# Kernel optimization log

Hardware: AMD Instinct MI355X
Metric: run time of the kernel (lower is better)

## Reference

```python
import jax, jax.numpy as jnp
import numpy as np

B, C, H, W = 8, 64, 256, 256


def setup_inputs() -> dict:
    key = jax.random.key(0)
    ks = jax.random.split(key, 7)
    return {
        "x": jax.random.normal(ks[0], (B, C, H, W), dtype=jnp.float32),
        "query_w": jax.random.normal(ks[1], (C, W, W), dtype=jnp.float32),
        "key_w": jax.random.normal(ks[2], (C, W, W), dtype=jnp.float32),
        "var_w": jax.random.normal(ks[3], (C, W, W), dtype=jnp.float32),
        "query_b": jax.random.normal(ks[4], (C, H, W), dtype=jnp.float32),
        "key_b": jax.random.normal(ks[5], (C, H, W), dtype=jnp.float32),
        "var_b": jax.random.normal(ks[6], (C, H, W), dtype=jnp.float32),
    }


def reference(x, query_w, key_w, var_w, query_b, key_b, var_b):
    # mode == 'horizontal': per-channel right-matmul over the W axis.
    # x: [B,C,H,W], *_w: [C,W,W] (broadcast over batch), *_b: [C,H,W].
    q = jnp.einsum("bchw,cwv->bchv", x, query_w) + query_b
    k = jnp.einsum("bchw,cwv->bchv", x, key_w) + key_b
    v = jnp.einsum("bchw,cwv->bchv", x, var_w) + var_b
    return jax.nn.softmax(q * k, axis=-1) * v
```

## Files before the change

kernel.cpp:

```cpp
#include <hip/hip_runtime.h>
#include <math.h>


#define Bn 8
#define Cn 64
#define Hn 256
#define Wn 256

typedef _Float16 f16x8 __attribute__((ext_vector_type(8)));
typedef _Float16 f16x4 __attribute__((ext_vector_type(4)));
typedef float    f32x16 __attribute__((ext_vector_type(16)));

#define MFMA(a, b, c) __builtin_amdgcn_mfma_f32_32x32x16_f16((a), (b), (c), 0, 0, 0)

#define LDS_ALO 2048
#define LDS_B   4096
#define LDS_SM  36864

__global__ __launch_bounds__(256, 2) void axile_attn_mfma3(
    const float* __restrict__ x,
    const float* __restrict__ wq,
    const float* __restrict__ wk,
    const float* __restrict__ wv,
    const float* __restrict__ bq,
    const float* __restrict__ bk,
    const float* __restrict__ bv,
    float* __restrict__ out)
{
    __shared__ __align__(16) char lds[38400];

    const int tid  = threadIdx.x;
    const int ncol = tid >> 6;
    const int lane = tid & 63;
    const int h    = lane >> 5;
    const int l31  = lane & 31;

    const int blk = blockIdx.x;
    const int c   = blk & 63;
    const int j   = blk >> 6;
    const int b   = j >> 2;
    const int h0  = (j & 3) * 64;

    const float* xbase = x + ((size_t)(b * Cn + c) * Hn + h0) * Wn;
    const float* w_q = wq + (size_t)c * Wn * Wn;
    const float* w_k = wk + (size_t)c * Wn * Wn;
    const float* w_v = wv + (size_t)c * Wn * Wn;

    const int n    = tid;
    const int ntW  = n >> 5;
    const int nl   = n & 31;
    const int am    = tid >> 2;
    const int akq   = tid & 3;
    const int amt   = am >> 5;
    const int alc   = ((akq >> 1) << 5) | (am & 31);
    const int aboff = (akq & 1) * 8;

    f32x16 accq[2][2], acck[2][2];
#pragma unroll
    for (int mt = 0; mt < 2; ++mt)
#pragma unroll
        for (int nt = 0; nt < 2; ++nt)
#pragma unroll
            for (int r = 0; r < 16; ++r) {
                accq[mt][nt][r] = 0.f;
                acck[mt][nt][r] = 0.f;
            }

    for (int kt = 0; kt < 16; ++kt) {
        const int k0 = kt * 16;
        __syncthreads();
#pragma unroll
        for (int mat = 0; mat < 2; ++mat) {
            const float* Wp = mat ? w_k : w_q;
            float w16[16];
#pragma unroll
            for (int r = 0; r < 16; ++r)
                w16[r] = Wp[(size_t)(k0 + r) * Wn + n];
            char* dplane = lds + LDS_B + (mat * 2) * 8192 + ntW * 1024;
#pragma unroll
            for (int h2 = 0; h2 < 2; ++h2) {
                f16x8 hi8, lo8;
#pragma unroll
                for (int e = 0; e < 8; ++e) {
                    const float wv_ = w16[h2 * 8 + e];
                    _Float16 hv = (_Float16)wv_;
                    hi8[e] = hv;
                    lo8[e] = (_Float16)(wv_ - (float)hv);
                }
                const int fo = ((h2 << 5) | nl) * 16;
                *(f16x8*)(dplane + fo) = hi8;
                *(f16x8*)(dplane + 8192 + fo) = lo8;
            }
        }
        {
            const float4 xx = *(const float4*)(xbase + (size_t)am * Wn + k0 + akq * 4);
            f16x4 hi4, lo4;
            _Float16 t0 = (_Float16)xx.x; hi4[0] = t0; lo4[0] = (_Float16)(xx.x - (float)t0);
            _Float16 t1 = (_Float16)xx.y; hi4[1] = t1; lo4[1] = (_Float16)(xx.y - (float)t1);
            _Float16 t2 = (_Float16)xx.z; hi4[2] = t2; lo4[2] = (_Float16)(xx.z - (float)t2);
            _Float16 t3 = (_Float16)xx.w; hi4[3] = t3; lo4[3] = (_Float16)(xx.w - (float)t3);
            *(f16x4*)(lds + amt * 1024 + alc * 16 + aboff) = hi4;
            *(f16x4*)(lds + LDS_ALO + amt * 1024 + alc * 16 + aboff) = lo4;
        }
        __syncthreads();

        f16x8 ah[2], al[2];
#pragma unroll
        for (int mt = 0; mt < 2; ++mt) {
            ah[mt] = *(const f16x8*)(lds + mt * 1024 + lane * 16);
            al[mt] = *(const f16x8*)(lds + LDS_ALO + mt * 1024 + lane * 16);
        }
#pragma unroll
        for (int nt = 0; nt < 2; ++nt) {
            const int ntile = ncol * 2 + nt;
            const char* bb = lds + LDS_B + ntile * 1024 + lane * 16;
            f16x8 bqh = *(const f16x8*)(bb + 0 * 8192);
            f16x8 bql = *(const f16x8*)(bb + 1 * 8192);
            f16x8 bkh = *(const f16x8*)(bb + 2 * 8192);
            f16x8 bkl = *(const f16x8*)(bb + 3 * 8192);
#pragma unroll
            for (int mt = 0; mt < 2; ++mt) {
                accq[mt][nt] = MFMA(ah[mt], bqh, accq[mt][nt]);
                accq[mt][nt] = MFMA(al[mt], bqh, accq[mt][nt]);
                accq[mt][nt] = MFMA(ah[mt], bql, accq[mt][nt]);
                acck[mt][nt] = MFMA(ah[mt], bkh, acck[mt][nt]);
                acck[mt][nt] = MFMA(al[mt], bkh, acck[mt][nt]);
                acck[mt][nt] = MFMA(ah[mt], bkl, acck[mt][nt]);
            }
        }
    }

    float* part    = (float*)(lds + LDS_SM);
    float* combmax = (float*)(lds + LDS_SM + 1024);
    float* combsum = (float*)(lds + LDS_SM + 1280);

#pragma unroll
    for (int mt = 0; mt < 2; ++mt)
#pragma unroll
        for (int nt = 0; nt < 2; ++nt)
#pragma unroll
            for (int r = 0; r < 16; ++r) {
                const int rl = (r & 3) + 8 * (r >> 2) + 4 * h;
                const int hh = h0 + mt * 32 + rl;
                const int vv = ncol * 64 + nt * 32 + l31;
                const size_t bidx = ((size_t)c * Hn + hh) * Wn + vv;
                const float qv = accq[mt][nt][r] + bq[bidx];
                const float kv = acck[mt][nt][r] + bk[bidx];
                accq[mt][nt][r] = qv * kv;
            }

#pragma unroll
    for (int mt = 0; mt < 2; ++mt)
#pragma unroll
        for (int r = 0; r < 16; ++r) {
            float m2 = fmaxf(accq[mt][0][r], accq[mt][1][r]);
#pragma unroll
            for (int off = 16; off > 0; off >>= 1)
                m2 = fmaxf(m2, __shfl_xor(m2, off, 64));
            if ((lane & 15) == r && ((lane >> 4) & 1) == mt) {
                const int rl  = (r & 3) + 8 * (r >> 2) + 4 * h;
                const int row = mt * 32 + rl;
                part[row * 4 + ncol] = m2;
            }
        }
    __syncthreads();
    if (tid < 64)
        combmax[tid] = fmaxf(fmaxf(part[tid * 4 + 0], part[tid * 4 + 1]),
                             fmaxf(part[tid * 4 + 2], part[tid * 4 + 3]));
    __syncthreads();

#pragma unroll
    for (int mt = 0; mt < 2; ++mt)
#pragma unroll
        for (int r = 0; r < 16; ++r) {
            const int rl  = (r & 3) + 8 * (r >> 2) + 4 * h;
            const int row = mt * 32 + rl;
            const float mx = combmax[row];
            const float e0 = __expf(accq[mt][0][r] - mx);
            const float e1 = __expf(accq[mt][1][r] - mx);
            accq[mt][0][r] = e0;
            accq[mt][1][r] = e1;
            float ps = e0 + e1;
#pragma unroll
            for (int off = 16; off > 0; off >>= 1)
                ps += __shfl_xor(ps, off, 64);
            if ((lane & 15) == r && ((lane >> 4) & 1) == mt)
                part[row * 4 + ncol] = ps;
        }
    __syncthreads();
    if (tid < 64)
        combsum[tid] = (part[tid * 4 + 0] + part[tid * 4 + 1]) +
                       (part[tid * 4 + 2] + part[tid * 4 + 3]);

    f32x16 accv[2][2];
#pragma unroll
    for (int mt = 0; mt < 2; ++mt)
#pragma unroll
        for (int nt = 0; nt < 2; ++nt)
#pragma unroll
            for (int r = 0; r < 16; ++r)
                accv[mt][nt][r] = 0.f;

    for (int kt = 0; kt < 16; ++kt) {
        const int k0 = kt * 16;
        __syncthreads();
        {
            float w16[16];
#pragma unroll
            for (int r = 0; r < 16; ++r)
                w16[r] = w_v[(size_t)(k0 + r) * Wn + n];
            char* dplane = lds + LDS_B + ntW * 1024;
#pragma unroll
            for (int h2 = 0; h2 < 2; ++h2) {
                f16x8 hi8;
#pragma unroll
                for (int e = 0; e < 8; ++e)
                    hi8[e] = (_Float16)w16[h2 * 8 + e];
                *(f16x8*)(dplane + ((h2 << 5) | nl) * 16) = hi8;
            }
        }
        {
            const float4 xx = *(const float4*)(xbase + (size_t)am * Wn + k0 + akq * 4);
            f16x4 hi4;
            hi4[0] = (_Float16)xx.x;
            hi4[1] = (_Float16)xx.y;
            hi4[2] = (_Float16)xx.z;
            hi4[3] = (_Float16)xx.w;
            *(f16x4*)(lds + amt * 1024 + alc * 16 + aboff) = hi4;
        }
        __syncthreads();

        f16x8 ah[2];
#pragma unroll
        for (int mt = 0; mt < 2; ++mt)
            ah[mt] = *(const f16x8*)(lds + mt * 1024 + lane * 16);
#pragma unroll
        for (int nt = 0; nt < 2; ++nt) {
            const int ntile = ncol * 2 + nt;
            f16x8 bvh = *(const f16x8*)(lds + LDS_B + ntile * 1024 + lane * 16);
#pragma unroll
            for (int mt = 0; mt < 2; ++mt)
                accv[mt][nt] = MFMA(ah[mt], bvh, accv[mt][nt]);
        }
    }

    float* obase = out + ((size_t)(b * Cn + c) * Hn) * Wn;
#pragma unroll
    for (int mt = 0; mt < 2; ++mt)
#pragma unroll
        for (int r = 0; r < 16; ++r) {
            const int rl  = (r & 3) + 8 * (r >> 2) + 4 * h;
            const int row = mt * 32 + rl;
            const float inv = 1.0f / combsum[row];
            const int hh = h0 + row;
#pragma unroll
            for (int nt = 0; nt < 2; ++nt) {
                const int vv = ncol * 64 + nt * 32 + l31;
                const size_t bidx = ((size_t)c * Hn + hh) * Wn + vv;
                const float vx = accv[mt][nt][r] + bv[bidx];
                obase[(size_t)hh * Wn + vv] = accq[mt][nt][r] * vx * inv;
            }
        }
}

extern "C" void kernel_launch(void* const* d_in, const int* in_sizes, int n_in,
                              void* d_out, int out_size, void* d_ws, size_t ws_size,
                              hipStream_t stream) {
    (void)in_sizes; (void)n_in; (void)out_size; (void)d_ws; (void)ws_size;
    const float* x  = (const float*)d_in[0];
    const float* wq = (const float*)d_in[1];
    const float* wk = (const float*)d_in[2];
    const float* wv = (const float*)d_in[3];
    const float* bq = (const float*)d_in[4];
    const float* bk = (const float*)d_in[5];
    const float* bv = (const float*)d_in[6];
    float* out = (float*)d_out;

    dim3 grid(Bn * 4 * Cn);
    dim3 block(256);
    hipLaunchKernelGGL(axile_attn_mfma3, grid, block, 0, stream,
                       x, wq, wk, wv, bq, bk, bv, out);
}
```

Baseline: 534.0 us.

## Pre-split weights to fp16 hi/lo MFMA layout once, load via global_load_lds

```diff
diff --git a/kernel.cpp b/kernel.cpp
--- a/kernel.cpp
+++ b/kernel.cpp
@@ -1,5 +1,6 @@
 #include <hip/hip_runtime.h>
 #include <math.h>
+#include <stdint.h>
 
 
 #define Bn 8
@@ -11,11 +12,275 @@
 typedef _Float16 f16x4 __attribute__((ext_vector_type(4)));
 typedef float    f32x16 __attribute__((ext_vector_type(16)));
 
+typedef __attribute__((address_space(1))) const uint32_t gl_u32;
+typedef __attribute__((address_space(3))) uint32_t lds_u32;
+
 #define MFMA(a, b, c) __builtin_amdgcn_mfma_f32_32x32x16_f16((a), (b), (c), 0, 0, 0)
+
+#define WP_PLANE 4096
+#define WP_CKT   (5 * WP_PLANE)
+#define WS_NEED  ((size_t)Cn * 16 * WP_CKT * sizeof(_Float16))
 
 #define LDS_ALO 2048
 #define LDS_B   4096
 #define LDS_SM  36864
+
+__global__ __launch_bounds__(256) void convert_w(
+    const float* __restrict__ wq,
+    const float* __restrict__ wk,
+    const float* __restrict__ wv,
+    _Float16* __restrict__ wc)
+{
+    const int gid   = blockIdx.x * 256 + threadIdx.x;
+    const int lane  = gid & 63;
+    const int ntile = (gid >> 6) & 7;
+    const int kt    = (gid >> 9) & 15;
+    const int c     = gid >> 13;
+
+    const int k0  = kt * 16 + (lane >> 5) * 8;
+    const int col = ntile * 32 + (lane & 31);
+    const size_t cb = (size_t)c * Wn * Wn;
+
+    _Float16* dst = wc + ((size_t)c * 16 + kt) * WP_CKT;
+    const int fo  = ntile * 512 + lane * 8;
+
+    f16x8 qh, ql, kh, kl, vh;
+#pragma unroll
+    for (int e = 0; e < 8; ++e) {
+        const size_t idx = cb + (size_t)(k0 + e) * Wn + col;
+        const float q = wq[idx];
+        const float k = wk[idx];
+        const float v = wv[idx];
+        _Float16 qhv = (_Float16)q;
+        _Float16 khv = (_Float16)k;
+        qh[e] = qhv; ql[e] = (_Float16)(q - (float)qhv);
+        kh[e] = khv; kl[e] = (_Float16)(k - (float)khv);
+        vh[e] = (_Float16)v;
+    }
+    *(f16x8*)(dst + 0 * WP_PLANE + fo) = qh;
+    *(f16x8*)(dst + 1 * WP_PLANE + fo) = ql;
+    *(f16x8*)(dst + 2 * WP_PLANE + fo) = kh;
+    *(f16x8*)(dst + 3 * WP_PLANE + fo) = kl;
+    *(f16x8*)(dst + 4 * WP_PLANE + fo) = vh;
+}
+
+__global__ __launch_bounds__(256, 2) void axile_attn_mfma4(
+    const float* __restrict__ x,
+    const _Float16* __restrict__ wc,
+    const float* __restrict__ bq,
+    const float* __restrict__ bk,
+    const float* __restrict__ bv,
+    float* __restrict__ out)
+{
+    __shared__ __align__(16) char lds[38400];
+
+    const int tid  = threadIdx.x;
+    const int ncol = tid >> 6;
+    const int lane = tid & 63;
+    const int h    = lane >> 5;
+    const int l31  = lane & 31;
+
+    const int blk = blockIdx.x;
+    const int c   = blk & 63;
+    const int j   = blk >> 6;
+    const int b   = j >> 2;
+    const int h0  = (j & 3) * 64;
+
+    const float* xbase = x + ((size_t)(b * Cn + c) * Hn + h0) * Wn;
+    const _Float16* wcc = wc + (size_t)c * 16 * WP_CKT;
+
+    const int am    = tid >> 2;
+    const int akq   = tid & 3;
+    const int alc   = ((akq >> 1) << 5) | (am & 31);
+    const int aboff = (akq & 1) * 8;
+    const int amt   = am >> 5;
+
+    f32x16 accq[2][2], acck[2][2];
+#pragma unroll
+    for (int mt = 0; mt < 2; ++mt)
+#pragma unroll
+        for (int nt = 0; nt < 2; ++nt)
+#pragma unroll
+            for (int r = 0; r < 16; ++r) {
+                accq[mt][nt][r] = 0.f;
+                acck[mt][nt][r] = 0.f;
+            }
+
+    for (int kt = 0; kt < 16; ++kt) {
+        const int k0 = kt * 16;
+        __syncthreads();
+        {
+            const _Float16* srcp = wcc + (size_t)kt * WP_CKT + ncol * WP_PLANE + lane * 8;
+            char* ldsp = lds + LDS_B + ncol * 8192;
+#pragma unroll
+            for (int nt8 = 0; nt8 < 8; ++nt8)
+                __builtin_amdgcn_global_load_lds(
+                    (gl_u32*)(srcp + nt8 * 512), (lds_u32*)(ldsp + nt8 * 1024), 16, 0, 0);
+        }
+        {
+            const float4 xx = *(const float4*)(xbase + (size_t)am * Wn + k0 + akq * 4);
+            f16x4 hi4, lo4;
+            _Float16 t0 = (_Float16)xx.x; hi4[0] = t0; lo4[0] = (_Float16)(xx.x - (float)t0);
+            _Float16 t1 = (_Float16)xx.y; hi4[1] = t1; lo4[1] = (_Float16)(xx.y - (float)t1);
+            _Float16 t2 = (_Float16)xx.z; hi4[2] = t2; lo4[2] = (_Float16)(xx.z - (float)t2);
+            _Float16 t3 = (_Float16)xx.w; hi4[3] = t3; lo4[3] = (_Float16)(xx.w - (float)t3);
+            *(f16x4*)(lds + amt * 1024 + alc * 16 + aboff) = hi4;
+            *(f16x4*)(lds + LDS_ALO + amt * 1024 + alc * 16 + aboff) = lo4;
+        }
+        __syncthreads();
+
+        f16x8 ah[2], al[2];
+#pragma unroll
+        for (int mt = 0; mt < 2; ++mt) {
+            ah[mt] = *(const f16x8*)(lds + mt * 1024 + lane * 16);
+            al[mt] = *(const f16x8*)(lds + LDS_ALO + mt * 1024 + lane * 16);
+        }
+#pragma unroll
+        for (int nt = 0; nt < 2; ++nt) {
+            const int ntile = ncol * 2 + nt;
+            const char* bb = lds + LDS_B + ntile * 1024 + lane * 16;
+            f16x8 bqh = *(const f16x8*)(bb + 0 * 8192);
+            f16x8 bql = *(const f16x8*)(bb + 1 * 8192);
+            f16x8 bkh = *(const f16x8*)(bb + 2 * 8192);
+            f16x8 bkl = *(const f16x8*)(bb + 3 * 8192);
+#pragma unroll
+            for (int mt = 0; mt < 2; ++mt) {
+                accq[mt][nt] = MFMA(ah[mt], bqh, accq[mt][nt]);
+                accq[mt][nt] = MFMA(al[mt], bqh, accq[mt][nt]);
+                accq[mt][nt] = MFMA(ah[mt], bql, accq[mt][nt]);
+                acck[mt][nt] = MFMA(ah[mt], bkh, acck[mt][nt]);
+                acck[mt][nt] = MFMA(al[mt], bkh, acck[mt][nt]);
+                acck[mt][nt] = MFMA(ah[mt], bkl, acck[mt][nt]);
+            }
+        }
+    }
+
+    float* part    = (float*)(lds + LDS_SM);
+    float* combmax = (float*)(lds + LDS_SM + 1024);
+    float* combsum = (float*)(lds + LDS_SM + 1280);
+
+#pragma unroll
+    for (int mt = 0; mt < 2; ++mt)
+#pragma unroll
+        for (int nt = 0; nt < 2; ++nt)
+#pragma unroll
+            for (int r = 0; r < 16; ++r) {
+                const int rl = (r & 3) + 8 * (r >> 2) + 4 * h;
+                const int hh = h0 + mt * 32 + rl;
+                const int vv = ncol * 64 + nt * 32 + l31;
+                const size_t bidx = ((size_t)c * Hn + hh) * Wn + vv;
+                const float qv = accq[mt][nt][r] + bq[bidx];
+                const float kv = acck[mt][nt][r] + bk[bidx];
+                accq[mt][nt][r] = qv * kv;
+            }
+
+#pragma unroll
+    for (int mt = 0; mt < 2; ++mt)
+#pragma unroll
+        for (int r = 0; r < 16; ++r) {
+            float m2 = fmaxf(accq[mt][0][r], accq[mt][1][r]);
+#pragma unroll
+            for (int off = 16; off > 0; off >>= 1)
+                m2 = fmaxf(m2, __shfl_xor(m2, off, 64));
+            if ((lane & 15) == r && ((lane >> 4) & 1) == mt) {
+                const int rl  = (r & 3) + 8 * (r >> 2) + 4 * h;
+                part[(mt * 32 + rl) * 4 + ncol] = m2;
+            }
+        }
+    __syncthreads();
+    if (tid < 64)
+        combmax[tid] = fmaxf(fmaxf(part[tid * 4 + 0], part[tid * 4 + 1]),
+                             fmaxf(part[tid * 4 + 2], part[tid * 4 + 3]));
+    __syncthreads();
+
+#pragma unroll
+    for (int mt = 0; mt < 2; ++mt)
+#pragma unroll
+        for (int r = 0; r < 16; ++r) {
+            const int rl  = (r & 3) + 8 * (r >> 2) + 4 * h;
+            const int row = mt * 32 + rl;
+            const float mx = combmax[row];
+            const float e0 = __expf(accq[mt][0][r] - mx);
+            const float e1 = __expf(accq[mt][1][r] - mx);
+            accq[mt][0][r] = e0;
+            accq[mt][1][r] = e1;
+            float ps = e0 + e1;
+#pragma unroll
+            for (int off = 16; off > 0; off >>= 1)
+                ps += __shfl_xor(ps, off, 64);
+            if ((lane & 15) == r && ((lane >> 4) & 1) == mt)
+                part[row * 4 + ncol] = ps;
+        }
+    __syncthreads();
+    if (tid < 64)
+        combsum[tid] = (part[tid * 4 + 0] + part[tid * 4 + 1]) +
+                       (part[tid * 4 + 2] + part[tid * 4 + 3]);
+
+    f32x16 accv[2][2];
+#pragma unroll
+    for (int mt = 0; mt < 2; ++mt)
+#pragma unroll
+        for (int nt = 0; nt < 2; ++nt)
+#pragma unroll
+            for (int r = 0; r < 16; ++r)
+                accv[mt][nt][r] = 0.f;
+
+    for (int kt = 0; kt < 16; ++kt) {
+        const int k0 = kt * 16;
+        __syncthreads();
+        {
+            const _Float16* srcp = wcc + (size_t)kt * WP_CKT + 4 * WP_PLANE + lane * 8;
+#pragma unroll
+            for (int i = 0; i < 2; ++i) {
+                const int nt8 = ncol * 2 + i;
+                __builtin_amdgcn_global_load_lds(
+                    (gl_u32*)(srcp + nt8 * 512),
+                    (lds_u32*)(lds + LDS_B + nt8 * 1024), 16, 0, 0);
+            }
+        }
+        {
+            const float4 xx = *(const float4*)(xbase + (size_t)am * Wn + k0 + akq * 4);
+            f16x4 hi4;
+            hi4[0] = (_Float16)xx.x;
+            hi4[1] = (_Float16)xx.y;
+            hi4[2] = (_Float16)xx.z;
+            hi4[3] = (_Float16)xx.w;
+            *(f16x4*)(lds + amt * 1024 + alc * 16 + aboff) = hi4;
+        }
+        __syncthreads();
+
+        f16x8 ah[2];
+#pragma unroll
+        for (int mt = 0; mt < 2; ++mt)
+            ah[mt] = *(const f16x8*)(lds + mt * 1024 + lane * 16);
+#pragma unroll
+        for (int nt = 0; nt < 2; ++nt) {
+            const int ntile = ncol * 2 + nt;
+            f16x8 bvh = *(const f16x8*)(lds + LDS_B + ntile * 1024 + lane * 16);
+#pragma unroll
+            for (int mt = 0; mt < 2; ++mt)
+                accv[mt][nt] = MFMA(ah[mt], bvh, accv[mt][nt]);
+        }
+    }
+
+    float* obase = out + ((size_t)(b * Cn + c) * Hn) * Wn;
+#pragma unroll
+    for (int mt = 0; mt < 2; ++mt)
+#pragma unroll
+        for (int r = 0; r < 16; ++r) {
+            const int rl  = (r & 3) + 8 * (r >> 2) + 4 * h;
+            const int row = mt * 32 + rl;
+            const float inv = 1.0f / combsum[row];
+            const int hh = h0 + row;
+#pragma unroll
+            for (int nt = 0; nt < 2; ++nt) {
+                const int vv = ncol * 64 + nt * 32 + l31;
+                const size_t bidx = ((size_t)c * Hn + hh) * Wn + vv;
+                const float vx = accv[mt][nt][r] + bv[bidx];
+                obase[(size_t)hh * Wn + vv] = accq[mt][nt][r] * vx * inv;
+            }
+        }
+}
 
 __global__ __launch_bounds__(256, 2) void axile_attn_mfma3(
     const float* __restrict__ x,
@@ -28,24 +293,20 @@
     float* __restrict__ out)
 {
     __shared__ __align__(16) char lds[38400];
-
     const int tid  = threadIdx.x;
     const int ncol = tid >> 6;
     const int lane = tid & 63;
     const int h    = lane >> 5;
     const int l31  = lane & 31;
-
     const int blk = blockIdx.x;
     const int c   = blk & 63;
     const int j   = blk >> 6;
     const int b   = j >> 2;
     const int h0  = (j & 3) * 64;
-
     const float* xbase = x + ((size_t)(b * Cn + c) * Hn + h0) * Wn;
     const float* w_q = wq + (size_t)c * Wn * Wn;
     const float* w_k = wk + (size_t)c * Wn * Wn;
     const float* w_v = wv + (size_t)c * Wn * Wn;
-
     const int n    = tid;
     const int ntW  = n >> 5;
     const int nl   = n & 31;
@@ -54,18 +315,13 @@
     const int amt   = am >> 5;
     const int alc   = ((akq >> 1) << 5) | (am & 31);
     const int aboff = (akq & 1) * 8;
-
     f32x16 accq[2][2], acck[2][2];
 #pragma unroll
     for (int mt = 0; mt < 2; ++mt)
 #pragma unroll
         for (int nt = 0; nt < 2; ++nt)
 #pragma unroll
-            for (int r = 0; r < 16; ++r) {
-                accq[mt][nt][r] = 0.f;
-                acck[mt][nt][r] = 0.f;
-            }
-
+            for (int r = 0; r < 16; ++r) { accq[mt][nt][r] = 0.f; acck[mt][nt][r] = 0.f; }
     for (int kt = 0; kt < 16; ++kt) {
         const int k0 = kt * 16;
         __syncthreads();
@@ -74,8 +330,7 @@
             const float* Wp = mat ? w_k : w_q;
             float w16[16];
 #pragma unroll
-            for (int r = 0; r < 16; ++r)
-                w16[r] = Wp[(size_t)(k0 + r) * Wn + n];
+            for (int r = 0; r < 16; ++r) w16[r] = Wp[(size_t)(k0 + r) * Wn + n];
             char* dplane = lds + LDS_B + (mat * 2) * 8192 + ntW * 1024;
 #pragma unroll
             for (int h2 = 0; h2 < 2; ++h2) {
@@ -84,8 +339,7 @@
                 for (int e = 0; e < 8; ++e) {
                     const float wv_ = w16[h2 * 8 + e];
                     _Float16 hv = (_Float16)wv_;
-                    hi8[e] = hv;
-                    lo8[e] = (_Float16)(wv_ - (float)hv);
+                    hi8[e] = hv; lo8[e] = (_Float16)(wv_ - (float)hv);
                 }
                 const int fo = ((h2 << 5) | nl) * 16;
                 *(f16x8*)(dplane + fo) = hi8;
@@ -103,7 +357,6 @@
             *(f16x4*)(lds + LDS_ALO + amt * 1024 + alc * 16 + aboff) = lo4;
         }
         __syncthreads();
-
         f16x8 ah[2], al[2];
 #pragma unroll
         for (int mt = 0; mt < 2; ++mt) {
@@ -129,11 +382,9 @@
             }
         }
     }
-
     float* part    = (float*)(lds + LDS_SM);
     float* combmax = (float*)(lds + LDS_SM + 1024);
     float* combsum = (float*)(lds + LDS_SM + 1280);
-
 #pragma unroll
     for (int mt = 0; mt < 2; ++mt)
 #pragma unroll
@@ -144,23 +395,18 @@
                 const int hh = h0 + mt * 32 + rl;
                 const int vv = ncol * 64 + nt * 32 + l31;
                 const size_t bidx = ((size_t)c * Hn + hh) * Wn + vv;
-                const float qv = accq[mt][nt][r] + bq[bidx];
-                const float kv = acck[mt][nt][r] + bk[bidx];
-                accq[mt][nt][r] = qv * kv;
-            }
-
+                accq[mt][nt][r] = (accq[mt][nt][r] + bq[bidx]) * (acck[mt][nt][r] + bk[bidx]);
+            }
 #pragma unroll
     for (int mt = 0; mt < 2; ++mt)
 #pragma unroll
         for (int r = 0; r < 16; ++r) {
             float m2 = fmaxf(accq[mt][0][r], accq[mt][1][r]);
 #pragma unroll
-            for (int off = 16; off > 0; off >>= 1)
-                m2 = fmaxf(m2, __shfl_xor(m2, off, 64));
+            for (int off = 16; off > 0; off >>= 1) m2 = fmaxf(m2, __shfl_xor(m2, off, 64));
             if ((lane & 15) == r && ((lane >> 4) & 1) == mt) {
                 const int rl  = (r & 3) + 8 * (r >> 2) + 4 * h;
-                const int row = mt * 32 + rl;
-                part[row * 4 + ncol] = m2;
+                part[(mt * 32 + rl) * 4 + ncol] = m2;
             }
         }
     __syncthreads();
@@ -168,7 +414,6 @@
         combmax[tid] = fmaxf(fmaxf(part[tid * 4 + 0], part[tid * 4 + 1]),
                              fmaxf(part[tid * 4 + 2], part[tid * 4 + 3]));
     __syncthreads();
-
 #pragma unroll
     for (int mt = 0; mt < 2; ++mt)
 #pragma unroll
@@ -178,72 +423,59 @@
             const float mx = combmax[row];
             const float e0 = __expf(accq[mt][0][r] - mx);
             const float e1 = __expf(accq[mt][1][r] - mx);
-            accq[mt][0][r] = e0;
-            accq[mt][1][r] = e1;
+            accq[mt][0][r] = e0; accq[mt][1][r] = e1;
             float ps = e0 + e1;
 #pragma unroll
-            for (int off = 16; off > 0; off >>= 1)
-                ps += __shfl_xor(ps, off, 64);
-            if ((lane & 15) == r && ((lane >> 4) & 1) == mt)
-                part[row * 4 + ncol] = ps;
+            for (int off = 16; off > 0; off >>= 1) ps += __shfl_xor(ps, off, 64);
+            if ((lane & 15) == r && ((lane >> 4) & 1) == mt) part[row * 4 + ncol] = ps;
         }
     __syncthreads();
     if (tid < 64)
         combsum[tid] = (part[tid * 4 + 0] + part[tid * 4 + 1]) +
                        (part[tid * 4 + 2] + part[tid * 4 + 3]);
-
     f32x16 accv[2][2];
 #pragma unroll
     for (int mt = 0; mt < 2; ++mt)
 #pragma unroll
         for (int nt = 0; nt < 2; ++nt)
 #pragma unroll
-            for (int r = 0; r < 16; ++r)
-                accv[mt][nt][r] = 0.f;
-
+            for (int r = 0; r < 16; ++r) accv[mt][nt][r] = 0.f;
     for (int kt = 0; kt < 16; ++kt) {
         const int k0 = kt * 16;
         __syncthreads();
         {
             float w16[16];
 #pragma unroll
-            for (int r = 0; r < 16; ++r)
-                w16[r] = w_v[(size_t)(k0 + r) * Wn + n];
+            for (int r = 0; r < 16; ++r) w16[r] = w_v[(size_t)(k0 + r) * Wn + n];
             char* dplane = lds + LDS_B + ntW * 1024;
 #pragma unroll
             for (int h2 = 0; h2 < 2; ++h2) {
                 f16x8 hi8;
 #pragma unroll
-                for (int e = 0; e < 8; ++e)
-                    hi8[e] = (_Float16)w16[h2 * 8 + e];
+                for (int e = 0; e < 8; ++e) hi8[e] = (_Float16)w16[h2 * 8 + e];
                 *(f16x8*)(dplane + ((h2 << 5) | nl) * 16) = hi8;
             }
         }
         {
             const float4 xx = *(const float4*)(xbase + (size_t)am * Wn + k0 + akq * 4);
             f16x4 hi4;
-            hi4[0] = (_Float16)xx.x;
-            hi4[1] = (_Float16)xx.y;
-            hi4[2] = (_Float16)xx.z;
-            hi4[3] = (_Float16)xx.w;
+            hi4[0] = (_Float16)xx.x; hi4[1] = (_Float16)xx.y;
+            hi4[2] = (_Float16)xx.z; hi4[3] = (_Float16)xx.w;
             *(f16x4*)(lds + amt * 1024 + alc * 16 + aboff) = hi4;
         }
         __syncthreads();
-
         f16x8 ah[2];
 #pragma unroll
         for (int mt = 0; mt < 2; ++mt)
             ah[mt] = *(const f16x8*)(lds + mt * 1024 + lane * 16);
 #pragma unroll
         for (int nt = 0; nt < 2; ++nt) {
-            const int ntile = ncol * 2 + nt;
-            f16x8 bvh = *(const f16x8*)(lds + LDS_B + ntile * 1024 + lane * 16);
+            f16x8 bvh = *(const f16x8*)(lds + LDS_B + (ncol * 2 + nt) * 1024 + lane * 16);
 #pragma unroll
             for (int mt = 0; mt < 2; ++mt)
                 accv[mt][nt] = MFMA(ah[mt], bvh, accv[mt][nt]);
         }
     }
-
     float* obase = out + ((size_t)(b * Cn + c) * Hn) * Wn;
 #pragma unroll
     for (int mt = 0; mt < 2; ++mt)
@@ -257,8 +489,7 @@
             for (int nt = 0; nt < 2; ++nt) {
                 const int vv = ncol * 64 + nt * 32 + l31;
                 const size_t bidx = ((size_t)c * Hn + hh) * Wn + vv;
-                const float vx = accv[mt][nt][r] + bv[bidx];
-                obase[(size_t)hh * Wn + vv] = accq[mt][nt][r] * vx * inv;
+                obase[(size_t)hh * Wn + vv] = accq[mt][nt][r] * (accv[mt][nt][r] + bv[bidx]) * inv;
             }
         }
 }
@@ -266,7 +497,7 @@
 extern "C" void kernel_launch(void* const* d_in, const int* in_sizes, int n_in,
                               void* d_out, int out_size, void* d_ws, size_t ws_size,
                               hipStream_t stream) {
-    (void)in_sizes; (void)n_in; (void)out_size; (void)d_ws; (void)ws_size;
+    (void)in_sizes; (void)n_in; (void)out_size;
     const float* x  = (const float*)d_in[0];
     const float* wq = (const float*)d_in[1];
     const float* wk = (const float*)d_in[2];
@@ -276,8 +507,13 @@
     const float* bv = (const float*)d_in[6];
     float* out = (float*)d_out;
 
-    dim3 grid(Bn * 4 * Cn);
-    dim3 block(256);
-    hipLaunchKernelGGL(axile_attn_mfma3, grid, block, 0, stream,
-                       x, wq, wk, wv, bq, bk, bv, out);
+    if (ws_size >= WS_NEED) {
+        _Float16* wc = (_Float16*)d_ws;
+        hipLaunchKernelGGL(convert_w, dim3(2048), dim3(256), 0, stream, wq, wk, wv, wc);
+        hipLaunchKernelGGL(axile_attn_mfma4, dim3(Bn * 4 * Cn), dim3(256), 0, stream,
+                           x, wc, bq, bk, bv, out);
+    } else {
+        hipLaunchKernelGGL(axile_attn_mfma3, dim3(Bn * 4 * Cn), dim3(256), 0, stream,
+                           x, wq, wk, wv, bq, bk, bv, out);
+    }
 }
```

Result: slower. 552.3 us (+3.4%).
